# Performance work log

Measured on AMD Instinct MI355X. Metric: run time of the kernel, lower is better.

## Reference

```python
import jax, jax.numpy as jnp
import numpy as np

B, S, E, H = 2, 2048, 1024, 16
HD = E // H
SCALE = 1.0 / np.sqrt(HD)
PR_QKV = 0.05   # precision_ratio for q/k/v (critical_attention=False)
PR_OUT = 0.10
ROUTE_THR = 0.05  # gradient_threshold (critical_attention=False)
LN_EPS = 1e-5


def rpb_linear(x, W, b, precision_ratio):
    """ResidualPrecisionBoostLinear: ternary-quantized weight (threshold 0.7*mean|W|,
    per-tensor scale) plus top-`precision_ratio` fraction of residual kept full precision."""
    absW = jnp.abs(W)
    thr = 0.7 * jnp.mean(absW)
    tmask = (absW > thr).astype(W.dtype)
    scale = jnp.sum(absW * tmask) / jnp.maximum(jnp.sum(tmask), 1.0)
    Wq = scale * jnp.sign(W) * tmask
    res = W - Wq
    k = int(precision_ratio * W.size)
    kth = jax.lax.top_k(jnp.abs(res).ravel(), k)[0][-1]
    W_eff = Wq + res * (jnp.abs(res) >= kth).astype(W.dtype)
    return x @ W_eff.T + b


def selective_route(x, threshold):
    # forward: zero out small-magnitude activations (straight-through in training)
    return x * (jnp.abs(x) >= threshold).astype(x.dtype)


def layer_norm(x, g, b):
    mu = jnp.mean(x, axis=-1, keepdims=True)
    var = jnp.mean(jnp.square(x - mu), axis=-1, keepdims=True)
    return (x - mu) * jax.lax.rsqrt(var + LN_EPS) * g + b


def setup_inputs() -> dict:
    key = jax.random.key(0)
    ks = jax.random.split(key, 12)
    f = lambda k, shp, s=1.0: jax.random.normal(k, shp, dtype=jnp.float32) * s
    return {
        "query": f(ks[0], (B, S, E)),
        "key": f(ks[1], (B, S, E)),
        "value": f(ks[2], (B, S, E)),
        "Wq": f(ks[3], (E, E), 0.02), "bq": jnp.zeros((E,), jnp.float32),
        "Wk": f(ks[4], (E, E), 0.02), "bk": jnp.zeros((E,), jnp.float32),
        "Wv": f(ks[5], (E, E), 0.02), "bv": jnp.zeros((E,), jnp.float32),
        "Wo": f(ks[6], (E, E), 0.02), "bo": jnp.zeros((E,), jnp.float32),
        "ln_g": jnp.ones((E,), jnp.float32),
        "ln_b": jnp.zeros((E,), jnp.float32),
    }


def reference(query, key, value, Wq, bq, Wk, bk, Wv, bv, Wo, bo, ln_g, ln_b):
    qn = layer_norm(query, ln_g, ln_b)
    q = selective_route(rpb_linear(qn, Wq, bq, PR_QKV), ROUTE_THR)
    k = selective_route(rpb_linear(key, Wk, bk, PR_QKV), ROUTE_THR)
    v = selective_route(rpb_linear(value, Wv, bv, PR_QKV), ROUTE_THR)
    # [B,S,E] -> [B,H,S,HD]
    q = q.reshape(B, S, H, HD).transpose(0, 2, 1, 3)
    k = k.reshape(B, S, H, HD).transpose(0, 2, 1, 3)
    v = v.reshape(B, S, H, HD).transpose(0, 2, 1, 3)
    scores = jnp.einsum("bhqd,bhkd->bhqk", q, k) * SCALE
    attn = jax.nn.softmax(scores, axis=-1)   # dropout is identity in eval
    ctx = jnp.einsum("bhqk,bhkd->bhqd", attn, v)
    ctx = ctx.transpose(0, 2, 1, 3).reshape(B, S, E)
    return rpb_linear(ctx, Wo, bo, PR_OUT)
```

## Files before the change

### kernel.cpp

```cpp
#include <hip/hip_runtime.h>
#include <stdio.h>
#include <stdint.h>

#define BB 2
#define SS 2048
#define ED 1024
#define HH 16
#define HDD 64
#define MROWS 4096
#define NW_ELEM 1048576u

typedef unsigned short ushortT;
typedef __attribute__((ext_vector_type(8))) short bf16x8;
typedef __attribute__((ext_vector_type(4))) float f32x4;
typedef __attribute__((ext_vector_type(16))) float f32x16;

#define U_WHI 0u
#define U_WLO 4194304u
#define U_AH  8388608u
#define U_AL  12582912u
#define U_BH  16777216u
#define U_BL  20971520u
#define U_QH  25165824u
#define U_QL  29360128u
#define U_KH  33554432u
#define U_KL  37748736u
#define U_VH  41943040u
#define U_VL  46137344u
#define SMALL_OFF  100663296u
#define HIST_OFF   SMALL_OFF
#define ABS_OFF    (SMALL_OFF + 16384u)
#define MSK_OFF    (ABS_OFF + 32u)
#define CNT_OFF    (MSK_OFF + 32u)
#define SMALL_BYTES 16464u
#define WS_NEEDED  (SMALL_OFF + SMALL_BYTES)

#define SC44 17592186044416.0f
#define INV44 (1.0 / 17592186044416.0)

__device__ __forceinline__ const float* wsel(int w, const float* W0, const float* W1,
                                             const float* W2, const float* W3) {
  return w == 0 ? W0 : w == 1 ? W1 : w == 2 ? W2 : W3;
}

__device__ __forceinline__ ushortT f2bf(float x) {
  unsigned u = __float_as_uint(x);
  unsigned r = (u + 0x7FFFu + ((u >> 16) & 1u)) >> 16;
  return (ushortT)r;
}
__device__ __forceinline__ float bf2f(ushortT b) {
  return __uint_as_float(((unsigned)b) << 16);
}
__device__ __forceinline__ void bsplit(float x, ushortT& h, ushortT& l) {
  ushortT hb = f2bf(x);
  float hf = bf2f(hb);
  h = hb;
  l = f2bf(x - hf);
}
__device__ __forceinline__ unsigned pkbf(float a, float b) {
  unsigned r;
  asm("v_cvt_pk_bf16_f32 %0, %1, %2" : "=v"(r) : "v"(a), "v"(b));
  return r;
}
__device__ __forceinline__ void plswap(unsigned& a, unsigned& b) {
  asm("v_permlane32_swap_b32 %0, %1" : "+v"(a), "+v"(b));
}

__device__ __forceinline__ void gld_lds16(const ushortT* g, ushortT* s) {
  __builtin_amdgcn_global_load_lds((__attribute__((address_space(1))) void*)g,
                                   (__attribute__((address_space(3))) void*)s, 16, 0, 0);
}

__device__ __forceinline__ float get_thr(const unsigned long long* sAbs, int w) {
  return 0.7f * (float)((double)sAbs[w] * INV44 / 1048576.0);
}
__device__ __forceinline__ float get_scale(const unsigned long long* sMsk,
                                           const unsigned* cnt, int w) {
  double s = (double)sMsk[w] * INV44;
  return (float)s / fmaxf((float)cnt[w], 1.0f);
}

__device__ __forceinline__ void scan_sel(const unsigned* hist, unsigned& k, unsigned& prefix,
                                         unsigned* sh, int t) {
  sh[t] = hist[t];
  __syncthreads();
  for (int off = 1; off < 256; off <<= 1) {
    unsigned add = (t + off < 256) ? sh[t + off] : 0u;
    __syncthreads();
    sh[t] += add;
    __syncthreads();
  }
  int sel = __syncthreads_count((int)(sh[t] >= k)) - 1;
  unsigned suf = sh[sel];
  k -= (suf - hist[sel]);
  prefix = (prefix << 8) | (unsigned)sel;
  __syncthreads();
}

__global__ __launch_bounds__(256) void k_wstats(const float* W0, const float* W1,
                                                const float* W2, const float* W3,
                                                unsigned long long* sAbs) {
  const int w = blockIdx.y, t = threadIdx.x;
  const float* W = wsel(w, W0, W1, W2, W3) + blockIdx.x * 4096;
  unsigned long long s = 0;
#pragma unroll
  for (int r = 0; r < 4; r++) {
    float4 v = *(const float4*)(W + (t + 256 * r) * 4);
    s += (unsigned long long)(fabsf(v.x) * SC44);
    s += (unsigned long long)(fabsf(v.y) * SC44);
    s += (unsigned long long)(fabsf(v.z) * SC44);
    s += (unsigned long long)(fabsf(v.w) * SC44);
  }
  __shared__ unsigned long long sd[256];
  sd[t] = s;
  __syncthreads();
  for (int off = 128; off > 0; off >>= 1) {
    if (t < off) sd[t] += sd[t + off];
    __syncthreads();
  }
  if (!t) atomicAdd(&sAbs[w], sd[0]);
}

__global__ __launch_bounds__(256) void k_masked(const float* W0, const float* W1,
                                                const float* W2, const float* W3,
                                                const unsigned long long* sAbs,
                                                unsigned long long* sMsk, unsigned* sCnt) {
  const int w = blockIdx.y, t = threadIdx.x;
  const float thr = get_thr(sAbs, w);
  const float* W = wsel(w, W0, W1, W2, W3) + blockIdx.x * 4096;
  unsigned long long s = 0;
  unsigned c = 0;
#pragma unroll
  for (int r = 0; r < 4; r++) {
    float4 v = *(const float4*)(W + (t + 256 * r) * 4);
    float xs[4] = {v.x, v.y, v.z, v.w};
#pragma unroll
    for (int q = 0; q < 4; q++) {
      float a = fabsf(xs[q]);
      if (a > thr) { s += (unsigned long long)(a * SC44); c++; }
    }
  }
  __shared__ unsigned long long sd[256];
  __shared__ unsigned sc[256];
  sd[t] = s; sc[t] = c;
  __syncthreads();
  for (int off = 128; off > 0; off >>= 1) {
    if (t < off) { sd[t] += sd[t + off]; sc[t] += sc[t + off]; }
    __syncthreads();
  }
  if (!t) { atomicAdd(&sMsk[w], sd[0]); atomicAdd(&sCnt[w], sc[0]); }
}

__global__ __launch_bounds__(256) void k_hist(const float* W0, const float* W1,
                                              const float* W2, const float* W3,
                                              const unsigned long long* sAbs,
                                              const unsigned long long* sMsk,
                                              const unsigned* sCnt,
                                              unsigned* histG, int pass) {
  const int w = blockIdx.y, t = threadIdx.x;
  __shared__ unsigned sh[256];
  __shared__ unsigned h[256];
  const float thr = get_thr(sAbs, w);
  const float scale = get_scale(sMsk, sCnt, w);
  unsigned k = (w == 3) ? 104857u : 52428u, prefix = 0u;
  for (int pp = 0; pp < pass; pp++)
    scan_sel(histG + (pp * 4 + w) * 256, k, prefix, sh, t);

  h[t] = 0;
  __syncthreads();
  const float* W = wsel(w, W0, W1, W2, W3) + blockIdx.x * 4096;
  const int shift1 = 32 - 8 * pass;
  const int shift2 = 24 - 8 * pass;
#pragma unroll
  for (int r = 0; r < 4; r++) {
    float4 v = *(const float4*)(W + (t + 256 * r) * 4);
    float xs[4] = {v.x, v.y, v.z, v.w};
#pragma unroll
    for (int q = 0; q < 4; q++) {
      float x = xs[q];
      float a = fabsf(x);
      float wq = (a > thr) ? copysignf(scale, x) : 0.0f;
      unsigned bits = __float_as_uint(fabsf(x - wq));
      if (pass == 0) {
        atomicAdd(&h[bits >> 24], 1u);
      } else {
        if ((bits >> shift1) == prefix)
          atomicAdd(&h[(bits >> shift2) & 255u], 1u);
      }
    }
  }
  __syncthreads();
  if (h[t]) atomicAdd(&histG[(pass * 4 + w) * 256 + t], h[t]);
}

__global__ __launch_bounds__(256) void k_weff(const float* W0, const float* W1,
                                              const float* W2, const float* W3,
                                              const unsigned long long* sAbs,
                                              const unsigned long long* sMsk,
                                              const unsigned* sCnt,
                                              const unsigned* histG,
                                              ushortT* Whi, ushortT* Wlo) {
  const int w = blockIdx.y, t = threadIdx.x;
  __shared__ unsigned sh[256];
  const float thr = get_thr(sAbs, w);
  const float scale = get_scale(sMsk, sCnt, w);
  unsigned k = (w == 3) ? 104857u : 52428u, kth = 0u;
  for (int pp = 0; pp < 4; pp++)
    scan_sel(histG + (pp * 4 + w) * 256, k, kth, sh, t);

  const unsigned idx = (blockIdx.x * 256 + t) * 4;
  const float* W = wsel(w, W0, W1, W2, W3);
  float4 v = *(const float4*)(W + idx);
  float xs[4] = {v.x, v.y, v.z, v.w};
  ushort4 h4, l4;
#pragma unroll
  for (int c = 0; c < 4; c++) {
    float x = xs[c];
    float a = fabsf(x);
    float wq = (a > thr) ? copysignf(scale, x) : 0.0f;
    float res = x - wq;
    unsigned bits = __float_as_uint(fabsf(res));
    float we = wq + ((bits >= kth) ? res : 0.0f);
    ushortT hh, ll;
    bsplit(we, hh, ll);
    ((ushortT*)&h4)[c] = hh;
    ((ushortT*)&l4)[c] = ll;
  }
  *(ushort4*)&Whi[(size_t)w * NW_ELEM + idx] = h4;
  *(ushort4*)&Wlo[(size_t)w * NW_ELEM + idx] = l4;
}

__global__ __launch_bounds__(256) void k_pre(const float* __restrict__ query,
                                             const float* __restrict__ key,
                                             const float* __restrict__ g,
                                             const float* __restrict__ b,
                                             ushortT* __restrict__ Ah, ushortT* __restrict__ Al,
                                             ushortT* __restrict__ Bh, ushortT* __restrict__ Bl) {
  const int t = threadIdx.x;
  if (blockIdx.y == 0) {
    const int row = blockIdx.x;
    __shared__ float red[8];
    float4 v = *(const float4*)&query[(size_t)row * ED + t * 4];
    float s = v.x + v.y + v.z + v.w;
#pragma unroll
    for (int m = 32; m; m >>= 1) s += __shfl_xor(s, m, 64);
    if ((t & 63) == 0) red[t >> 6] = s;
    __syncthreads();
    float mu = (red[0] + red[1] + red[2] + red[3]) * (1.0f / 1024.0f);
    float dx = v.x - mu, dy = v.y - mu, dz = v.z - mu, dw = v.w - mu;
    float s2 = dx * dx + dy * dy + dz * dz + dw * dw;
#pragma unroll
    for (int m = 32; m; m >>= 1) s2 += __shfl_xor(s2, m, 64);
    if ((t & 63) == 0) red[4 + (t >> 6)] = s2;
    __syncthreads();
    float var = (red[4] + red[5] + red[6] + red[7]) * (1.0f / 1024.0f);
    float inv = rsqrtf(var + 1e-5f);
    float4 gg = *(const float4*)&g[t * 4];
    float4 bb = *(const float4*)&b[t * 4];
    float ys[4] = {dx * inv * gg.x + bb.x, dy * inv * gg.y + bb.y,
                   dz * inv * gg.z + bb.z, dw * inv * gg.w + bb.w};
    ushort4 h4, l4;
#pragma unroll
    for (int c = 0; c < 4; c++) {
      ushortT hh, ll;
      bsplit(ys[c], hh, ll);
      ((ushortT*)&h4)[c] = hh;
      ((ushortT*)&l4)[c] = ll;
    }
    *(ushort4*)&Ah[(size_t)row * ED + t * 4] = h4;
    *(ushort4*)&Al[(size_t)row * ED + t * 4] = l4;
  } else {
    const int i = (blockIdx.x * 256 + t) * 4;
    float4 v = *(const float4*)&key[i];
    float xs[4] = {v.x, v.y, v.z, v.w};
    ushort4 h4, l4;
#pragma unroll
    for (int c = 0; c < 4; c++) {
      ushortT hh, ll;
      bsplit(xs[c], hh, ll);
      ((ushortT*)&h4)[c] = hh;
      ((ushortT*)&l4)[c] = ll;
    }
    *(ushort4*)&Bh[i] = h4;
    *(ushort4*)&Bl[i] = l4;
  }
}

__global__ __launch_bounds__(256) void k_splitv(const float* __restrict__ X,
                                                ushortT* __restrict__ H,
                                                ushortT* __restrict__ L) {
  const int i = (blockIdx.x * 256 + threadIdx.x) * 4;
  float4 v = *(const float4*)&X[i];
  float xs[4] = {v.x, v.y, v.z, v.w};
  ushort4 h4, l4;
#pragma unroll
  for (int c = 0; c < 4; c++) {
    ushortT hh, ll;
    bsplit(xs[c], hh, ll);
    ((ushortT*)&h4)[c] = hh;
    ((ushortT*)&l4)[c] = ll;
  }
  *(ushort4*)&H[i] = h4;
  *(ushort4*)&L[i] = l4;
}

__device__ __forceinline__ f32x4 mfma16(bf16x8 a, bf16x8 b, f32x4 c) {
  return __builtin_amdgcn_mfma_f32_16x16x32_bf16(a, b, c, 0, 0, 0);
}

template <int MODE>
__global__ __launch_bounds__(256, 2) void k_gemm_mfma(
    const ushortT* __restrict__ Ah, const ushortT* __restrict__ Al,
    const ushortT* __restrict__ Wh, const ushortT* __restrict__ Wl,
    const float* __restrict__ bias, void* Cp, void* C2p) {
  __shared__ __align__(16) ushortT sAh[8192], sAl[8192];
  __shared__ __align__(16) ushortT sBh[4096], sBl[4096];
  const int t = threadIdx.x;
  const int w = t >> 6, l = t & 63;
  const int wr = w >> 1, wc = w & 1;

  int id = blockIdx.x;
  int id2 = (id & 7) * 64 + (id >> 3);
  const int mt = id2 >> 4, nt = id2 & 15;
  const int m0 = mt * 128, n0 = nt * 64;

  f32x4 acc[4][2];
#pragma unroll
  for (int i = 0; i < 4; i++)
#pragma unroll
    for (int j = 0; j < 2; j++) acc[i][j] = (f32x4){0.0f, 0.0f, 0.0f, 0.0f};

  const int sr = l >> 3, sg = l & 7;
  const int swz = sg ^ sr;

  for (int kt = 0; kt < 16; ++kt) {
    __syncthreads();
#pragma unroll
    for (int s2 = 0; s2 < 4; s2++) {
      int seg = w * 4 + s2;
      size_t g = (size_t)(m0 + seg * 8 + sr) * ED + kt * 64 + swz * 8;
      gld_lds16(Ah + g, sAh + seg * 512);
      gld_lds16(Al + g, sAl + seg * 512);
    }
#pragma unroll
    for (int s2 = 0; s2 < 2; s2++) {
      int seg = w * 2 + s2;
      size_t g = (size_t)(n0 + seg * 8 + sr) * ED + kt * 64 + swz * 8;
      gld_lds16(Wh + g, sBh + seg * 512);
      gld_lds16(Wl + g, sBl + seg * 512);
    }
    __syncthreads();
#pragma unroll
    for (int ks = 0; ks < 2; ks++) {
      bf16x8 ah[4], al[4], bh[2], bl[2];
      const int G = ks * 4 + (l >> 4);
#pragma unroll
      for (int i = 0; i < 4; i++) {
        int r = wr * 64 + i * 16 + (l & 15);
        int off = r * 64 + ((G ^ (l & 7)) << 3);
        ah[i] = *(const bf16x8*)&sAh[off];
        al[i] = *(const bf16x8*)&sAl[off];
      }
#pragma unroll
      for (int j = 0; j < 2; j++) {
        int r = wc * 32 + j * 16 + (l & 15);
        int off = r * 64 + ((G ^ (l & 7)) << 3);
        bh[j] = *(const bf16x8*)&sBh[off];
        bl[j] = *(const bf16x8*)&sBl[off];
      }
#pragma unroll
      for (int i = 0; i < 4; i++)
#pragma unroll
        for (int j = 0; j < 2; j++) {
          acc[i][j] = mfma16(ah[i], bh[j], acc[i][j]);
          acc[i][j] = mfma16(ah[i], bl[j], acc[i][j]);
          acc[i][j] = mfma16(al[i], bh[j], acc[i][j]);
        }
    }
  }

  const int coln = l & 15, row4 = (l >> 4) * 4;
  float bn[2];
#pragma unroll
  for (int j = 0; j < 2; j++) bn[j] = bias[n0 + wc * 32 + j * 16 + coln];

  if (MODE == 1) {
    float* C = (float*)Cp;
#pragma unroll
    for (int i = 0; i < 4; i++)
#pragma unroll
      for (int j = 0; j < 2; j++) {
        int n = n0 + wc * 32 + j * 16 + coln;
#pragma unroll
        for (int r = 0; r < 4; r++) {
          int m = m0 + wr * 64 + i * 16 + row4 + r;
          C[(size_t)m * ED + n] = acc[i][j][r] + bn[j];
        }
      }
  } else if (MODE == 0) {
    ushortT* Ch = (ushortT*)Cp;
    ushortT* Cl = (ushortT*)C2p;
    const int b_ = m0 >> 11, h_ = n0 >> 6;
#pragma unroll
    for (int i = 0; i < 4; i++)
#pragma unroll
      for (int j = 0; j < 2; j++) {
        int hd = wc * 32 + j * 16 + coln;
#pragma unroll
        for (int r = 0; r < 4; r++) {
          int m = m0 + wr * 64 + i * 16 + row4 + r;
          int s_ = m & 2047;
          float y = acc[i][j][r] + bn[j];
          y = (fabsf(y) >= 0.05f) ? y : 0.0f;
          ushortT hh, ll;
          bsplit(y, hh, ll);
          size_t idx = ((size_t)(b_ * HH + h_) * SS + s_) * HDD + hd;
          Ch[idx] = hh;
          Cl[idx] = ll;
        }
      }
  } else {
    ushortT* Ch = (ushortT*)Cp;
    ushortT* Cl = (ushortT*)C2p;
    const int b_ = m0 >> 11, h_ = n0 >> 6;
#pragma unroll
    for (int i = 0; i < 4; i++)
#pragma unroll
      for (int j = 0; j < 2; j++) {
        int hd = wc * 32 + j * 16 + coln;
        int s0_ = (m0 + wr * 64 + i * 16 + row4) & 2047;
        ushort4 h4, l4;
#pragma unroll
        for (int r = 0; r < 4; r++) {
          float y = acc[i][j][r] + bn[j];
          y = (fabsf(y) >= 0.05f) ? y : 0.0f;
          ushortT hh, ll;
          bsplit(y, hh, ll);
          ((ushortT*)&h4)[r] = hh;
          ((ushortT*)&l4)[r] = ll;
        }
        size_t idx = ((size_t)(b_ * HH + h_) * HDD + hd) * SS + s0_;
        *(ushort4*)&Ch[idx] = h4;
        *(ushort4*)&Cl[idx] = l4;
      }
  }
}

__device__ __forceinline__ f32x16 mfma32(bf16x8 a, bf16x8 b, f32x16 c) {
  return __builtin_amdgcn_mfma_f32_32x32x16_bf16(a, b, c, 0, 0, 0);
}

__device__ __forceinline__ void exppack(const f32x16& A, float EC, float& lsum,
                                        bf16x8& paA, bf16x8& paB) {
  float p[16];
#pragma unroll
  for (int r = 0; r < 16; r++) {
    p[r] = exp2f(A[r] * EC);
    lsum += p[r];
  }
  unsigned c0 = pkbf(p[0], p[1]), c1 = pkbf(p[2], p[3]);
  unsigned c2 = pkbf(p[4], p[5]), c3 = pkbf(p[6], p[7]);
  unsigned c4 = pkbf(p[8], p[9]), c5 = pkbf(p[10], p[11]);
  unsigned c6 = pkbf(p[12], p[13]), c7 = pkbf(p[14], p[15]);
  plswap(c0, c2); plswap(c1, c3); plswap(c4, c6); plswap(c5, c7);
  uint4 ta = make_uint4(c0, c1, c2, c3);
  uint4 tb = make_uint4(c4, c5, c6, c7);
  paA = __builtin_bit_cast(bf16x8, ta);
  paB = __builtin_bit_cast(bf16x8, tb);
}

__global__ __launch_bounds__(256, 3) void k_attn(
    const ushortT* __restrict__ Qh, const ushortT* __restrict__ Ql,
    const ushortT* __restrict__ Kh,
    const ushortT* __restrict__ Vh, const ushortT* __restrict__ Vl,
    ushortT* __restrict__ ctxH, ushortT* __restrict__ ctxL) {
  __shared__ __align__(16) ushortT sKh[4096];
  __shared__ __align__(16) ushortT sVh[4096], sVl[4096];

  const int t = threadIdx.x;
  const int w = t >> 6, l = t & 63;
  const int l32 = l & 31, g = l >> 5;

  int id = blockIdx.x;
  int id2 = (id & 7) * 64 + (id >> 3);
  const int bh = id2 >> 4, qt = id2 & 15;

  const size_t kqbase = (size_t)bh * (SS * HDD);
  const size_t vbase = (size_t)bh * (HDD * SS);
  const int q0 = qt * 128 + w * 32;

  bf16x8 qh[4], ql[4];
  const size_t qrow = kqbase + (size_t)(q0 + l32) * HDD;
#pragma unroll
  for (int ks = 0; ks < 4; ks++) {
    int d0 = ks * 16 + g * 8;
    qh[ks] = *(const bf16x8*)&Qh[qrow + d0];
    ql[ks] = *(const bf16x8*)&Ql[qrow + d0];
  }

  f32x16 octx0, octx1;
#pragma unroll
  for (int i = 0; i < 16; i++) { octx0[i] = 0.0f; octx1[i] = 0.0f; }
  float lsum = 0.0f;

  const float EC = 0.125f * 1.44269504088896f;

  const int srow = l >> 3;
  const int sgr = (l & 7) ^ srow;

  for (int kt = 0; kt < 32; ++kt) {
    const int s0 = kt * 64;
    __syncthreads();
#pragma unroll
    for (int s2 = 0; s2 < 2; s2++) {
      int seg = w * 2 + s2;
      int row = seg * 8 + srow;
      gld_lds16(Kh + kqbase + (size_t)(s0 + row) * HDD + sgr * 8, sKh + seg * 512);
      gld_lds16(Vh + vbase + (size_t)row * SS + s0 + sgr * 8, sVh + seg * 512);
      gld_lds16(Vl + vbase + (size_t)row * SS + s0 + sgr * 8, sVl + seg * 512);
    }
    __syncthreads();

    f32x16 acc0, acc1;
#pragma unroll
    for (int i = 0; i < 16; i++) { acc0[i] = 0.0f; acc1[i] = 0.0f; }
#pragma unroll
    for (int ks = 0; ks < 4; ks++) {
      int sw = ((ks * 2 + g) ^ (l32 & 7)) << 3;
      bf16x8 kh0 = *(const bf16x8*)&sKh[l32 * 64 + sw];
      bf16x8 kh1 = *(const bf16x8*)&sKh[(32 + l32) * 64 + sw];
      acc0 = mfma32(kh0, qh[ks], acc0);
      acc0 = mfma32(kh0, ql[ks], acc0);
      acc1 = mfma32(kh1, qh[ks], acc1);
      acc1 = mfma32(kh1, ql[ks], acc1);
    }

    bf16x8 pa0, pa1, pa2, pa3;
    exppack(acc0, EC, lsum, pa0, pa1);
    exppack(acc1, EC, lsum, pa2, pa3);

#pragma unroll
    for (int js = 0; js < 4; js++) {
      bf16x8 pj = js == 0 ? pa0 : js == 1 ? pa1 : js == 2 ? pa2 : pa3;
      int vsw = ((js * 2 + g) ^ (l32 & 7)) << 3;
      bf16x8 vh0 = *(const bf16x8*)&sVh[l32 * 64 + vsw];
      bf16x8 vl0 = *(const bf16x8*)&sVl[l32 * 64 + vsw];
      bf16x8 vh1 = *(const bf16x8*)&sVh[(32 + l32) * 64 + vsw];
      bf16x8 vl1 = *(const bf16x8*)&sVl[(32 + l32) * 64 + vsw];
      octx0 = mfma32(pj, vh0, octx0);
      octx0 = mfma32(pj, vl0, octx0);
      octx1 = mfma32(pj, vh1, octx1);
      octx1 = mfma32(pj, vl1, octx1);
    }
  }

  float ls = lsum + __shfl_xor(lsum, 32, 64);

  const int b_ = bh >> 4, h_ = bh & 15;
#pragma unroll
  for (int r = 0; r < 16; r++) {
    int q = (r & 3) + 8 * (r >> 2) + 4 * g;
    float inv = 1.0f / __shfl(ls, q, 64);
    size_t base = ((size_t)(b_ * SS + q0 + q)) * ED + h_ * HDD;
    ushortT hh, ll;
    bsplit(octx0[r] * inv, hh, ll);
    ctxH[base + l32] = hh;
    ctxL[base + l32] = ll;
    bsplit(octx1[r] * inv, hh, ll);
    ctxH[base + 32 + l32] = hh;
    ctxL[base + 32 + l32] = ll;
  }
}

extern "C" void kernel_launch(void* const* d_in, const int* in_sizes, int n_in,
                              void* d_out, int out_size, void* d_ws, size_t ws_size,
                              hipStream_t stream) {
  const float* query = (const float*)d_in[0];
  const float* key   = (const float*)d_in[1];
  const float* value = (const float*)d_in[2];
  const float* Wq = (const float*)d_in[3];
  const float* bq = (const float*)d_in[4];
  const float* Wk = (const float*)d_in[5];
  const float* bk = (const float*)d_in[6];
  const float* Wv = (const float*)d_in[7];
  const float* bv = (const float*)d_in[8];
  const float* Wo = (const float*)d_in[9];
  const float* bo = (const float*)d_in[10];
  const float* lng = (const float*)d_in[11];
  const float* lnb = (const float*)d_in[12];
  float* out = (float*)d_out;

  if (ws_size < (size_t)WS_NEEDED) {
    fprintf(stderr, "kernel_launch: ws too small (%zu < %u)\n", ws_size, WS_NEEDED);
    return;
  }

  ushortT* wsu = (ushortT*)d_ws;
  ushortT* Whi = wsu + U_WHI;
  ushortT* Wlo = wsu + U_WLO;
  ushortT* Abh = wsu + U_AH;
  ushortT* Abl = wsu + U_AL;
  ushortT* Bbh = wsu + U_BH;
  ushortT* Bbl = wsu + U_BL;
  ushortT* Qhp = wsu + U_QH;
  ushortT* Qlp = wsu + U_QL;
  ushortT* Khp = wsu + U_KH;
  ushortT* Klp = wsu + U_KL;
  ushortT* Vhp = wsu + U_VH;
  ushortT* Vlp = wsu + U_VL;

  char* wsb = (char*)d_ws;
  unsigned* histG = (unsigned*)(wsb + HIST_OFF);
  unsigned long long* sAbs = (unsigned long long*)(wsb + ABS_OFF);
  unsigned long long* sMsk = (unsigned long long*)(wsb + MSK_OFF);
  unsigned* sCnt = (unsigned*)(wsb + CNT_OFF);

  hipMemsetAsync(histG, 0, SMALL_BYTES, stream);

  dim3 gW(256, 4);
  k_wstats<<<gW, 256, 0, stream>>>(Wq, Wk, Wv, Wo, sAbs);
  k_masked<<<gW, 256, 0, stream>>>(Wq, Wk, Wv, Wo, sAbs, sMsk, sCnt);
  for (int pass = 0; pass < 4; ++pass)
    k_hist<<<gW, 256, 0, stream>>>(Wq, Wk, Wv, Wo, sAbs, sMsk, sCnt, histG, pass);
  k_weff<<<dim3(1024, 4), 256, 0, stream>>>(Wq, Wk, Wv, Wo, sAbs, sMsk, sCnt, histG,
                                            Whi, Wlo);

  k_pre<<<dim3(MROWS, 2), 256, 0, stream>>>(query, key, lng, lnb, Abh, Abl, Bbh, Bbl);

  k_gemm_mfma<0><<<512, 256, 0, stream>>>(Abh, Abl, Whi + 0 * NW_ELEM, Wlo + 0 * NW_ELEM,
                                          bq, Qhp, Qlp);
  k_gemm_mfma<0><<<512, 256, 0, stream>>>(Bbh, Bbl, Whi + 1 * NW_ELEM, Wlo + 1 * NW_ELEM,
                                          bk, Khp, Klp);
  k_splitv<<<4096, 256, 0, stream>>>(value, Abh, Abl);
  k_gemm_mfma<2><<<512, 256, 0, stream>>>(Abh, Abl, Whi + 2 * NW_ELEM, Wlo + 2 * NW_ELEM,
                                          bv, Vhp, Vlp);

  k_attn<<<512, 256, 0, stream>>>(Qhp, Qlp, Khp, Vhp, Vlp, Abh, Abl);

  k_gemm_mfma<1><<<512, 256, 0, stream>>>(Abh, Abl, Whi + 3 * NW_ELEM, Wlo + 3 * NW_ELEM,
                                          bo, out, nullptr);
}
```

Measured before the change: 293.6 us.

## Drop bf16 low-part splits for Q/K/V paths and double-buffer GEMM and attention tiles

Replaces the hi/lo bf16 split emulation with a single bf16 operand for the Q and K projections, the V-projection activations, and the QK^T and PV products in attention. This cuts MFMA count and memory traffic by roughly a third to a half in those stages. The full split is kept only for the output projection and the V weights. It also adds LDS double buffering to the GEMM and attention loops so loads overlap compute. The cost is lower numerical precision, which risks failing tolerance, and more LDS use, which cuts attention occupancy from 3 to 2 blocks.

```diff
diff --git a/kernel.cpp b/kernel.cpp
--- a/kernel.cpp
+++ b/kernel.cpp
@@ -18,16 +18,13 @@
 #define U_WHI 0u
 #define U_WLO 4194304u
 #define U_AH  8388608u
-#define U_AL  12582912u
-#define U_BH  16777216u
-#define U_BL  20971520u
-#define U_QH  25165824u
-#define U_QL  29360128u
-#define U_KH  33554432u
-#define U_KL  37748736u
-#define U_VH  41943040u
-#define U_VL  46137344u
-#define SMALL_OFF  100663296u
+#define U_BH  12582912u
+#define U_QH  16777216u
+#define U_KH  20971520u
+#define U_VH  25165824u
+#define U_CH  29360128u
+#define U_CL  33554432u
+#define SMALL_OFF  75497472u
 #define HIST_OFF   SMALL_OFF
 #define ABS_OFF    (SMALL_OFF + 16384u)
 #define MSK_OFF    (ABS_OFF + 32u)
@@ -234,8 +231,8 @@
                                              const float* __restrict__ key,
                                              const float* __restrict__ g,
                                              const float* __restrict__ b,
-                                             ushortT* __restrict__ Ah, ushortT* __restrict__ Al,
-                                             ushortT* __restrict__ Bh, ushortT* __restrict__ Bl) {
+                                             ushortT* __restrict__ Ah,
+                                             ushortT* __restrict__ Bh) {
   const int t = threadIdx.x;
   if (blockIdx.y == 0) {
     const int row = blockIdx.x;
@@ -259,62 +256,42 @@
     float4 bb = *(const float4*)&b[t * 4];
     float ys[4] = {dx * inv * gg.x + bb.x, dy * inv * gg.y + bb.y,
                    dz * inv * gg.z + bb.z, dw * inv * gg.w + bb.w};
-    ushort4 h4, l4;
-#pragma unroll
-    for (int c = 0; c < 4; c++) {
-      ushortT hh, ll;
-      bsplit(ys[c], hh, ll);
-      ((ushortT*)&h4)[c] = hh;
-      ((ushortT*)&l4)[c] = ll;
-    }
+    ushort4 h4;
+#pragma unroll
+    for (int c = 0; c < 4; c++) ((ushortT*)&h4)[c] = f2bf(ys[c]);
     *(ushort4*)&Ah[(size_t)row * ED + t * 4] = h4;
-    *(ushort4*)&Al[(size_t)row * ED + t * 4] = l4;
   } else {
     const int i = (blockIdx.x * 256 + t) * 4;
     float4 v = *(const float4*)&key[i];
-    float xs[4] = {v.x, v.y, v.z, v.w};
-    ushort4 h4, l4;
-#pragma unroll
-    for (int c = 0; c < 4; c++) {
-      ushortT hh, ll;
-      bsplit(xs[c], hh, ll);
-      ((ushortT*)&h4)[c] = hh;
-      ((ushortT*)&l4)[c] = ll;
-    }
+    ushort4 h4;
+    h4.x = f2bf(v.x); h4.y = f2bf(v.y); h4.z = f2bf(v.z); h4.w = f2bf(v.w);
     *(ushort4*)&Bh[i] = h4;
-    *(ushort4*)&Bl[i] = l4;
-  }
-}
-
-__global__ __launch_bounds__(256) void k_splitv(const float* __restrict__ X,
-                                                ushortT* __restrict__ H,
-                                                ushortT* __restrict__ L) {
+  }
+}
+
+__global__ __launch_bounds__(256) void k_splith(const float* __restrict__ X,
+                                                ushortT* __restrict__ H) {
   const int i = (blockIdx.x * 256 + threadIdx.x) * 4;
   float4 v = *(const float4*)&X[i];
-  float xs[4] = {v.x, v.y, v.z, v.w};
-  ushort4 h4, l4;
-#pragma unroll
-  for (int c = 0; c < 4; c++) {
-    ushortT hh, ll;
-    bsplit(xs[c], hh, ll);
-    ((ushortT*)&h4)[c] = hh;
-    ((ushortT*)&l4)[c] = ll;
-  }
+  ushort4 h4;
+  h4.x = f2bf(v.x); h4.y = f2bf(v.y); h4.z = f2bf(v.z); h4.w = f2bf(v.w);
   *(ushort4*)&H[i] = h4;
-  *(ushort4*)&L[i] = l4;
 }
 
 __device__ __forceinline__ f32x4 mfma16(bf16x8 a, bf16x8 b, f32x4 c) {
   return __builtin_amdgcn_mfma_f32_16x16x32_bf16(a, b, c, 0, 0, 0);
 }
 
-template <int MODE>
-__global__ __launch_bounds__(256, 2) void k_gemm_mfma(
+template <int MODE, bool ALO, bool WLO, bool DBUF>
+__global__ __launch_bounds__(256, 2) void k_gemm(
     const ushortT* __restrict__ Ah, const ushortT* __restrict__ Al,
     const ushortT* __restrict__ Wh, const ushortT* __restrict__ Wl,
-    const float* __restrict__ bias, void* Cp, void* C2p) {
-  __shared__ __align__(16) ushortT sAh[8192], sAl[8192];
-  __shared__ __align__(16) ushortT sBh[4096], sBl[4096];
+    const float* __restrict__ bias, ushortT* Cp, float* Cf) {
+  constexpr int NB = DBUF ? 2 : 1;
+  __shared__ __align__(16) ushortT sAh[NB * 8192];
+  __shared__ __align__(16) ushortT sAl[ALO ? NB * 8192 : 8];
+  __shared__ __align__(16) ushortT sBh[NB * 4096];
+  __shared__ __align__(16) ushortT sBl[WLO ? NB * 4096 : 8];
   const int t = threadIdx.x;
   const int w = t >> 6, l = t & 63;
   const int wr = w >> 1, wc = w & 1;
@@ -324,32 +301,33 @@
   const int mt = id2 >> 4, nt = id2 & 15;
   const int m0 = mt * 128, n0 = nt * 64;
 
-  f32x4 acc[4][2];
-#pragma unroll
-  for (int i = 0; i < 4; i++)
-#pragma unroll
-    for (int j = 0; j < 2; j++) acc[i][j] = (f32x4){0.0f, 0.0f, 0.0f, 0.0f};
-
   const int sr = l >> 3, sg = l & 7;
   const int swz = sg ^ sr;
 
-  for (int kt = 0; kt < 16; ++kt) {
-    __syncthreads();
+  auto stage = [&](int kt, int buf) {
 #pragma unroll
     for (int s2 = 0; s2 < 4; s2++) {
       int seg = w * 4 + s2;
       size_t g = (size_t)(m0 + seg * 8 + sr) * ED + kt * 64 + swz * 8;
-      gld_lds16(Ah + g, sAh + seg * 512);
-      gld_lds16(Al + g, sAl + seg * 512);
+      gld_lds16(Ah + g, sAh + buf * 8192 + seg * 512);
+      if constexpr (ALO) gld_lds16(Al + g, sAl + buf * 8192 + seg * 512);
     }
 #pragma unroll
     for (int s2 = 0; s2 < 2; s2++) {
       int seg = w * 2 + s2;
       size_t g = (size_t)(n0 + seg * 8 + sr) * ED + kt * 64 + swz * 8;
-      gld_lds16(Wh + g, sBh + seg * 512);
-      gld_lds16(Wl + g, sBl + seg * 512);
-    }
-    __syncthreads();
+      gld_lds16(Wh + g, sBh + buf * 4096 + seg * 512);
+      if constexpr (WLO) gld_lds16(Wl + g, sBl + buf * 4096 + seg * 512);
+    }
+  };
+
+  f32x4 acc[4][2];
+#pragma unroll
+  for (int i = 0; i < 4; i++)
+#pragma unroll
+    for (int j = 0; j < 2; j++) acc[i][j] = (f32x4){0.0f, 0.0f, 0.0f, 0.0f};
+
+  auto compute = [&](int buf) {
 #pragma unroll
     for (int ks = 0; ks < 2; ks++) {
       bf16x8 ah[4], al[4], bh[2], bl[2];
@@ -357,25 +335,42 @@
 #pragma unroll
       for (int i = 0; i < 4; i++) {
         int r = wr * 64 + i * 16 + (l & 15);
-        int off = r * 64 + ((G ^ (l & 7)) << 3);
+        int off = buf * 8192 + r * 64 + ((G ^ (l & 7)) << 3);
         ah[i] = *(const bf16x8*)&sAh[off];
-        al[i] = *(const bf16x8*)&sAl[off];
+        if constexpr (ALO) al[i] = *(const bf16x8*)&sAl[off];
       }
 #pragma unroll
       for (int j = 0; j < 2; j++) {
         int r = wc * 32 + j * 16 + (l & 15);
-        int off = r * 64 + ((G ^ (l & 7)) << 3);
+        int off = buf * 4096 + r * 64 + ((G ^ (l & 7)) << 3);
         bh[j] = *(const bf16x8*)&sBh[off];
-        bl[j] = *(const bf16x8*)&sBl[off];
+        if constexpr (WLO) bl[j] = *(const bf16x8*)&sBl[off];
       }
 #pragma unroll
       for (int i = 0; i < 4; i++)
 #pragma unroll
         for (int j = 0; j < 2; j++) {
           acc[i][j] = mfma16(ah[i], bh[j], acc[i][j]);
-          acc[i][j] = mfma16(ah[i], bl[j], acc[i][j]);
-          acc[i][j] = mfma16(al[i], bh[j], acc[i][j]);
+          if constexpr (WLO) acc[i][j] = mfma16(ah[i], bl[j], acc[i][j]);
+          if constexpr (ALO) acc[i][j] = mfma16(al[i], bh[j], acc[i][j]);
         }
+    }
+  };
+
+  if constexpr (DBUF) {
+    stage(0, 0);
+    __syncthreads();
+    for (int kt = 0; kt < 16; ++kt) {
+      if (kt < 15) stage(kt + 1, (kt + 1) & 1);
+      compute(kt & 1);
+      __syncthreads();
+    }
+  } else {
+    for (int kt = 0; kt < 16; ++kt) {
+      __syncthreads();
+      stage(kt, 0);
+      __syncthreads();
+      compute(0);
     }
   }
 
@@ -384,8 +379,7 @@
 #pragma unroll
   for (int j = 0; j < 2; j++) bn[j] = bias[n0 + wc * 32 + j * 16 + coln];
 
-  if (MODE == 1) {
-    float* C = (float*)Cp;
+  if constexpr (MODE == 1) {
 #pragma unroll
     for (int i = 0; i < 4; i++)
 #pragma unroll
@@ -394,12 +388,10 @@
 #pragma unroll
         for (int r = 0; r < 4; r++) {
           int m = m0 + wr * 64 + i * 16 + row4 + r;
-          C[(size_t)m * ED + n] = acc[i][j][r] + bn[j];
+          Cf[(size_t)m * ED + n] = acc[i][j][r] + bn[j];
         }
       }
-  } else if (MODE == 0) {
-    ushortT* Ch = (ushortT*)Cp;
-    ushortT* Cl = (ushortT*)C2p;
+  } else if constexpr (MODE == 0) {
     const int b_ = m0 >> 11, h_ = n0 >> 6;
 #pragma unroll
     for (int i = 0; i < 4; i++)
@@ -412,16 +404,10 @@
           int s_ = m & 2047;
           float y = acc[i][j][r] + bn[j];
           y = (fabsf(y) >= 0.05f) ? y : 0.0f;
-          ushortT hh, ll;
-          bsplit(y, hh, ll);
-          size_t idx = ((size_t)(b_ * HH + h_) * SS + s_) * HDD + hd;
-          Ch[idx] = hh;
-          Cl[idx] = ll;
+          Cp[((size_t)(b_ * HH + h_) * SS + s_) * HDD + hd] = f2bf(y);
         }
       }
   } else {
-    ushortT* Ch = (ushortT*)Cp;
-    ushortT* Cl = (ushortT*)C2p;
     const int b_ = m0 >> 11, h_ = n0 >> 6;
 #pragma unroll
     for (int i = 0; i < 4; i++)
@@ -429,19 +415,14 @@
       for (int j = 0; j < 2; j++) {
         int hd = wc * 32 + j * 16 + coln;
         int s0_ = (m0 + wr * 64 + i * 16 + row4) & 2047;
-        ushort4 h4, l4;
+        ushort4 h4;
 #pragma unroll
         for (int r = 0; r < 4; r++) {
           float y = acc[i][j][r] + bn[j];
           y = (fabsf(y) >= 0.05f) ? y : 0.0f;
-          ushortT hh, ll;
-          bsplit(y, hh, ll);
-          ((ushortT*)&h4)[r] = hh;
-          ((ushortT*)&l4)[r] = ll;
+          ((ushortT*)&h4)[r] = f2bf(y);
         }
-        size_t idx = ((size_t)(b_ * HH + h_) * HDD + hd) * SS + s0_;
-        *(ushort4*)&Ch[idx] = h4;
-        *(ushort4*)&Cl[idx] = l4;
+        *(ushort4*)&Cp[((size_t)(b_ * HH + h_) * HDD + hd) * SS + s0_] = h4;
       }
   }
 }
@@ -469,13 +450,12 @@
   paB = __builtin_bit_cast(bf16x8, tb);
 }
 
-__global__ __launch_bounds__(256, 3) void k_attn(
-    const ushortT* __restrict__ Qh, const ushortT* __restrict__ Ql,
-    const ushortT* __restrict__ Kh,
-    const ushortT* __restrict__ Vh, const ushortT* __restrict__ Vl,
+__global__ __launch_bounds__(256, 2) void k_attn(
+    const ushortT* __restrict__ Qh, const ushortT* __restrict__ Kh,
+    const ushortT* __restrict__ Vh,
     ushortT* __restrict__ ctxH, ushortT* __restrict__ ctxL) {
-  __shared__ __align__(16) ushortT sKh[4096];
-  __shared__ __align__(16) ushortT sVh[4096], sVl[4096];
+  __shared__ __align__(16) ushortT sK[2 * 4096];
+  __shared__ __align__(16) ushortT sV[2 * 4096];
 
   const int t = threadIdx.x;
   const int w = t >> 6, l = t & 63;
@@ -489,14 +469,10 @@
   const size_t vbase = (size_t)bh * (HDD * SS);
   const int q0 = qt * 128 + w * 32;
 
-  bf16x8 qh[4], ql[4];
+  bf16x8 qh[4];
   const size_t qrow = kqbase + (size_t)(q0 + l32) * HDD;
 #pragma unroll
-  for (int ks = 0; ks < 4; ks++) {
-    int d0 = ks * 16 + g * 8;
-    qh[ks] = *(const bf16x8*)&Qh[qrow + d0];
-    ql[ks] = *(const bf16x8*)&Ql[qrow + d0];
-  }
+  for (int ks = 0; ks < 4; ks++) qh[ks] = *(const bf16x8*)&Qh[qrow + ks * 16 + g * 8];
 
   f32x16 octx0, octx1;
 #pragma unroll
@@ -508,18 +484,24 @@
   const int srow = l >> 3;
   const int sgr = (l & 7) ^ srow;
 
-  for (int kt = 0; kt < 32; ++kt) {
+  auto stageA = [&](int kt, int buf) {
     const int s0 = kt * 64;
-    __syncthreads();
 #pragma unroll
     for (int s2 = 0; s2 < 2; s2++) {
       int seg = w * 2 + s2;
       int row = seg * 8 + srow;
-      gld_lds16(Kh + kqbase + (size_t)(s0 + row) * HDD + sgr * 8, sKh + seg * 512);
-      gld_lds16(Vh + vbase + (size_t)row * SS + s0 + sgr * 8, sVh + seg * 512);
-      gld_lds16(Vl + vbase + (size_t)row * SS + s0 + sgr * 8, sVl + seg * 512);
-    }
-    __syncthreads();
+      gld_lds16(Kh + kqbase + (size_t)(s0 + row) * HDD + sgr * 8, sK + buf * 4096 + seg * 512);
+      gld_lds16(Vh + vbase + (size_t)row * SS + s0 + sgr * 8, sV + buf * 4096 + seg * 512);
+    }
+  };
+
+  stageA(0, 0);
+  __syncthreads();
+
+  for (int kt = 0; kt < 32; ++kt) {
+    if (kt < 31) stageA(kt + 1, (kt + 1) & 1);
+    const ushortT* cK = sK + (kt & 1) * 4096;
+    const ushortT* cV = sV + (kt & 1) * 4096;
 
     f32x16 acc0, acc1;
 #pragma unroll
@@ -527,12 +509,10 @@
 #pragma unroll
     for (int ks = 0; ks < 4; ks++) {
       int sw = ((ks * 2 + g) ^ (l32 & 7)) << 3;
-      bf16x8 kh0 = *(const bf16x8*)&sKh[l32 * 64 + sw];
-      bf16x8 kh1 = *(const bf16x8*)&sKh[(32 + l32) * 64 + sw];
+      bf16x8 kh0 = *(const bf16x8*)&cK[l32 * 64 + sw];
+      bf16x8 kh1 = *(const bf16x8*)&cK[(32 + l32) * 64 + sw];
       acc0 = mfma32(kh0, qh[ks], acc0);
-      acc0 = mfma32(kh0, ql[ks], acc0);
       acc1 = mfma32(kh1, qh[ks], acc1);
-      acc1 = mfma32(kh1, ql[ks], acc1);
     }
 
     bf16x8 pa0, pa1, pa2, pa3;
@@ -543,15 +523,12 @@
     for (int js = 0; js < 4; js++) {
       bf16x8 pj = js == 0 ? pa0 : js == 1 ? pa1 : js == 2 ? pa2 : pa3;
       int vsw = ((js * 2 + g) ^ (l32 & 7)) << 3;
-      bf16x8 vh0 = *(const bf16x8*)&sVh[l32 * 64 + vsw];
-      bf16x8 vl0 = *(const bf16x8*)&sVl[l32 * 64 + vsw];
-      bf16x8 vh1 = *(const bf16x8*)&sVh[(32 + l32) * 64 + vsw];
-      bf16x8 vl1 = *(const bf16x8*)&sVl[(32 + l32) * 64 + vsw];
+      bf16x8 vh0 = *(const bf16x8*)&cV[l32 * 64 + vsw];
+      bf16x8 vh1 = *(const bf16x8*)&cV[(32 + l32) * 64 + vsw];
       octx0 = mfma32(pj, vh0, octx0);
-      octx0 = mfma32(pj, vl0, octx0);
       octx1 = mfma32(pj, vh1, octx1);
-      octx1 = mfma32(pj, vl1, octx1);
-    }
+    }
+    __syncthreads();
   }
 
   float ls = lsum + __shfl_xor(lsum, 32, 64);
@@ -599,15 +576,12 @@
   ushortT* Whi = wsu + U_WHI;
   ushortT* Wlo = wsu + U_WLO;
   ushortT* Abh = wsu + U_AH;
-  ushortT* Abl = wsu + U_AL;
   ushortT* Bbh = wsu + U_BH;
-  ushortT* Bbl = wsu + U_BL;
   ushortT* Qhp = wsu + U_QH;
-  ushortT* Qlp = wsu + U_QL;
   ushortT* Khp = wsu + U_KH;
-  ushortT* Klp = wsu + U_KL;
   ushortT* Vhp = wsu + U_VH;
-  ushortT* Vlp = wsu + U_VL;
+  ushortT* Chp = wsu + U_CH;
+  ushortT* Clp = wsu + U_CL;
 
   char* wsb = (char*)d_ws;
   unsigned* histG = (unsigned*)(wsb + HIST_OFF);
@@ -625,18 +599,19 @@
   k_weff<<<dim3(1024, 4), 256, 0, stream>>>(Wq, Wk, Wv, Wo, sAbs, sMsk, sCnt, histG,
                                             Whi, Wlo);
 
-  k_pre<<<dim3(MROWS, 2), 256, 0, stream>>>(query, key, lng, lnb, Abh, Abl, Bbh, Bbl);
-
-  k_gemm_mfma<0><<<512, 256, 0, stream>>>(Abh, Abl, Whi + 0 * NW_ELEM, Wlo + 0 * NW_ELEM,
-                                          bq, Qhp, Qlp);
-  k_gemm_mfma<0><<<512, 256, 0, stream>>>(Bbh, Bbl, Whi + 1 * NW_ELEM, Wlo + 1 * NW_ELEM,
-                                          bk, Khp, Klp);
-  k_splitv<<<4096, 256, 0, stream>>>(value, Abh, Abl);
-  k_gemm_mfma<2><<<512, 256, 0, stream>>>(Abh, Abl, Whi + 2 * NW_ELEM, Wlo + 2 * NW_ELEM,
-                                          bv, Vhp, Vlp);
-
-  k_attn<<<512, 256, 0, stream>>>(Qhp, Qlp, Khp, Vhp, Vlp, Abh, Abl);
-
-  k_gemm_mfma<1><<<512, 256, 0, stream>>>(Abh, Abl, Whi + 3 * NW_ELEM, Wlo + 3 * NW_ELEM,
-                                          bo, out, nullptr);
-}
+  k_pre<<<dim3(MROWS, 2), 256, 0, stream>>>(query, key, lng, lnb, Abh, Bbh);
+
+  k_gemm<0, false, false, true><<<512, 256, 0, stream>>>(
+      Abh, nullptr, Whi + 0 * NW_ELEM, nullptr, bq, Qhp, nullptr);
+  k_gemm<0, false, false, true><<<512, 256, 0, stream>>>(
+      Bbh, nullptr, Whi + 1 * NW_ELEM, nullptr, bk, Khp, nullptr);
+
+  k_splith<<<4096, 256, 0, stream>>>(value, Abh);
+  k_gemm<2, false, true, true><<<512, 256, 0, stream>>>(
+      Abh, nullptr, Whi + 2 * NW_ELEM, Wlo + 2 * NW_ELEM, bv, Vhp, nullptr);
+
+  k_attn<<<512, 256, 0, stream>>>(Qhp, Khp, Vhp, Chp, Clp);
+
+  k_gemm<1, true, true, false><<<512, 256, 0, stream>>>(
+      Chp, Clp, Whi + 3 * NW_ELEM, Wlo + 3 * NW_ELEM, bo, nullptr, out);
+}
```

Result: faster. 257.1 us (-12.4%).
